# Optimization experiments

Hardware: AMD Instinct MI355X
Metric: run time of the kernel (lower is better)

## Reference

```python
import jax, jax.numpy as jnp
import numpy as np

HIDDEN = 1024
FEAT = 2048
BOTTLENECK = 512
B, T = 64, 512


def setup_inputs() -> dict:
    key = jax.random.key(0)
    k1, k2, k3, k4, k5 = jax.random.split(key, 5)
    hidden = jax.random.normal(k1, (B, HIDDEN), dtype=jnp.float32)
    feats = jax.random.normal(k2, (B, T, FEAT), dtype=jnp.float32)
    # nn.Linear weights stored as [out, in]; apply as x @ W.T
    W = jax.random.normal(k3, (BOTTLENECK, HIDDEN), dtype=jnp.float32) * (1.0 / np.sqrt(HIDDEN))
    U = jax.random.normal(k4, (BOTTLENECK, FEAT), dtype=jnp.float32) * (1.0 / np.sqrt(FEAT))
    b = jnp.ones((BOTTLENECK,), dtype=jnp.float32)
    w = jax.random.normal(k5, (1, BOTTLENECK), dtype=jnp.float32) * (1.0 / np.sqrt(BOTTLENECK))
    return {"hidden": hidden, "feats": feats, "W": W, "U": U, "b": b, "w": w}


def reference(hidden, feats, W, U, b, w):
    Wh = hidden @ W.T                      # [B, K]
    Uv = jnp.einsum('btf,kf->btk', feats, U)  # [B, T, K]
    e = jnp.tanh(Wh[:, None, :] + Uv + b)  # [B, T, K]
    energies = jnp.einsum('btk,ok->bto', e, w)  # [B, T, 1]
    weights = jax.nn.softmax(energies, axis=1)  # softmax over time
    attn_feats = jnp.sum(feats * weights, axis=1)  # [B, F]
    return attn_feats, weights
```

## Files before the change

kernel.cpp:

```cpp
#include <hip/hip_runtime.h>
#include <hip/hip_bf16.h>
#include <math.h>

#define BATCH 64
#define TDIM 512
#define FEAT 2048
#define HID 1024
#define KDIM 512
#define MROWS (BATCH * TDIM)
#define TCH 16
#define TCLEN (TDIM / TCH)

#define FEATS4 (MROWS * FEAT / 4)
#define U4 (KDIM * FEAT / 4)

typedef __attribute__((ext_vector_type(8))) short short8;
typedef __attribute__((ext_vector_type(4))) float floatx4;

#define GLL16(g, l)                                                     \
    __builtin_amdgcn_global_load_lds(                                   \
        (const __attribute__((address_space(1))) void*)(g),             \
        (__attribute__((address_space(3))) void*)(l), 16, 0, 0)

__device__ __forceinline__ unsigned short f2bf(float x) {
    unsigned int u = __float_as_uint(x);
    u += 0x7FFFu + ((u >> 16) & 1u);
    return (unsigned short)(u >> 16);
}

__device__ __forceinline__ float bf2f(unsigned short s) {
    return __uint_as_float(((unsigned int)s) << 16);
}

__global__ __launch_bounds__(256) void k0_fused(const float* __restrict__ feats,
                                                const float* __restrict__ U,
                                                const float* __restrict__ hidden,
                                                const float* __restrict__ W,
                                                const float* __restrict__ bias,
                                                unsigned short* __restrict__ fB,
                                                unsigned short* __restrict__ uB,
                                                float* __restrict__ whb) {
    int bx = blockIdx.x;
    if (bx < 1792) {
        int stride = 1792 * 256;
        for (int i = bx * 256 + threadIdx.x; i < FEATS4; i += stride) {
            float4 v = ((const float4*)feats)[i];
            ushort4 o;
            o.x = f2bf(v.x); o.y = f2bf(v.y); o.z = f2bf(v.z); o.w = f2bf(v.w);
            ((ushort4*)fB)[i] = o;
        }
    } else if (bx < 2048) {
        int stride = 256 * 256;
        for (int i = (bx - 1792) * 256 + threadIdx.x; i < U4; i += stride) {
            float4 v = ((const float4*)U)[i];
            ushort4 o;
            o.x = f2bf(v.x); o.y = f2bf(v.y); o.z = f2bf(v.z); o.w = f2bf(v.w);
            ((ushort4*)uB)[i] = o;
        }
    } else {
        int bid = bx - 2048;
        int b = bid >> 7;
        int k = (bid & 127) * 4 + (threadIdx.x >> 6);
        int lane = threadIdx.x & 63;
        const float* hrow = hidden + (size_t)b * HID;
        const float* wrow = W + (size_t)k * HID;
        float acc = 0.f;
        #pragma unroll 4
        for (int h = lane; h < HID; h += 64) acc += hrow[h] * wrow[h];
        #pragma unroll
        for (int off = 32; off > 0; off >>= 1) acc += __shfl_down(acc, off, 64);
        if (lane == 0) whb[b * KDIM + k] = acc + bias[k];
    }
}

__global__ __launch_bounds__(256, 2) void k2_mfma(const unsigned short* __restrict__ fB,
                                                  const unsigned short* __restrict__ uB,
                                                  const float* __restrict__ whb,
                                                  const float* __restrict__ wvec,
                                                  float* __restrict__ partial) {
    __shared__ unsigned short As[256 * 64];
    __shared__ unsigned short Bs[128 * 64];
    __shared__ float sums[2][256];

    const int tid  = threadIdx.x;
    const int wave = tid >> 6;
    const int lane = tid & 63;
    const int row0 = blockIdx.x * 256;
    const int k0   = blockIdx.y * 128;
    const int wm = wave >> 1, wn = wave & 1;
    const int col = lane & 15, quad = lane >> 4;

    const unsigned short* gA[8];
    unsigned short* lA[8];
    #pragma unroll
    for (int g = 0; g < 8; ++g) {
        int s = wave * 512 + g * 64 + lane;
        int r = s >> 3;
        int q = (s & 7) ^ (r & 7);
        gA[g] = fB + (size_t)(row0 + r) * FEAT + q * 8;
        lA[g] = As + (wave * 512 + g * 64) * 8;
    }
    const unsigned short* gBp[4];
    unsigned short* lB[4];
    #pragma unroll
    for (int g = 0; g < 4; ++g) {
        int s = wave * 256 + g * 64 + lane;
        int r = s >> 3;
        int q = (s & 7) ^ (r & 7);
        gBp[g] = uB + (size_t)(k0 + r) * FEAT + q * 8;
        lB[g] = Bs + (wave * 256 + g * 64) * 8;
    }

    floatx4 acc[8][4];
    #pragma unroll
    for (int i = 0; i < 8; ++i)
        #pragma unroll
        for (int j = 0; j < 4; ++j) acc[i][j] = (floatx4){0.f, 0.f, 0.f, 0.f};

    for (int f0 = 0; f0 < FEAT; f0 += 64) {
        #pragma unroll
        for (int g = 0; g < 8; ++g) { GLL16(gA[g], lA[g]); gA[g] += 64; }
        #pragma unroll
        for (int g = 0; g < 4; ++g) { GLL16(gBp[g], lB[g]); gBp[g] += 64; }
        __syncthreads();

        #pragma unroll
        for (int kk = 0; kk < 2; ++kk) {
            const int sw = ((kk * 4 + quad) ^ (col & 7)) * 8;
            short8 af[8], bf[4];
            #pragma unroll
            for (int i = 0; i < 8; ++i)
                af[i] = *(const short8*)&As[(wm * 128 + i * 16 + col) * 64 + sw];
            #pragma unroll
            for (int j = 0; j < 4; ++j)
                bf[j] = *(const short8*)&Bs[(wn * 64 + j * 16 + col) * 64 + sw];
            #pragma unroll
            for (int i = 0; i < 8; ++i)
                #pragma unroll
                for (int j = 0; j < 4; ++j)
                    acc[i][j] = __builtin_amdgcn_mfma_f32_16x16x32_bf16(
                        af[i], bf[j], acc[i][j], 0, 0, 0);
        }
        __syncthreads();
    }

    const int b = row0 >> 9;
    float wk[4], hk[4];
    #pragma unroll
    for (int j = 0; j < 4; ++j) {
        int k = k0 + wn * 64 + j * 16 + col;
        wk[j] = wvec[k];
        hk[j] = whb[b * KDIM + k];
    }
    #pragma unroll
    for (int i = 0; i < 8; ++i) {
        #pragma unroll
        for (int r = 0; r < 4; ++r) {
            float s = 0.f;
            #pragma unroll
            for (int j = 0; j < 4; ++j)
                s += tanhf(acc[i][j][r] + hk[j]) * wk[j];
            #pragma unroll
            for (int off = 8; off > 0; off >>= 1)
                s += __shfl_down(s, off, 16);
            if (col == 0)
                sums[wn][wm * 128 + i * 16 + quad * 4 + r] = s;
        }
    }
    __syncthreads();
    partial[blockIdx.y * MROWS + row0 + tid] = sums[0][tid] + sums[1][tid];
}

#define BM 128
#define BN 128
#define BF 16
#define LDSPAD 4

__global__ __launch_bounds__(256) void k2_energy(const float* __restrict__ feats,
                                                 const float* __restrict__ U,
                                                 const float* __restrict__ whb,
                                                 const float* __restrict__ wvec,
                                                 float* __restrict__ partial) {
    __shared__ __align__(16) float As[BF][BM + LDSPAD];
    __shared__ __align__(16) float Us[BF][BN + LDSPAD];

    const int row0 = blockIdx.x * BM;
    const int k0   = blockIdx.y * BN;
    const int tid  = threadIdx.x;
    const int tx   = tid & 15;
    const int ty   = tid >> 4;

    float acc[8][8];
    #pragma unroll
    for (int i = 0; i < 8; ++i)
        #pragma unroll
        for (int j = 0; j < 8; ++j) acc[i][j] = 0.f;

    for (int f0 = 0; f0 < FEAT; f0 += BF) {
        #pragma unroll
        for (int l = 0; l < 2; ++l) {
            int li = tid + l * 256;
            int r  = li >> 2;
            int c4 = (li & 3) * 4;
            float4 av = *(const float4*)(feats + (size_t)(row0 + r) * FEAT + f0 + c4);
            float4 uv = *(const float4*)(U     + (size_t)(k0   + r) * FEAT + f0 + c4);
            As[c4 + 0][r] = av.x; As[c4 + 1][r] = av.y;
            As[c4 + 2][r] = av.z; As[c4 + 3][r] = av.w;
            Us[c4 + 0][r] = uv.x; Us[c4 + 1][r] = uv.y;
            Us[c4 + 2][r] = uv.z; Us[c4 + 3][r] = uv.w;
        }
        __syncthreads();
        #pragma unroll
        for (int kf = 0; kf < BF; ++kf) {
            float4 a0 = *(const float4*)&As[kf][ty * 8];
            float4 a1 = *(const float4*)&As[kf][ty * 8 + 4];
            float4 u0 = *(const float4*)&Us[kf][tx * 8];
            float4 u1 = *(const float4*)&Us[kf][tx * 8 + 4];
            float a[8] = {a0.x, a0.y, a0.z, a0.w, a1.x, a1.y, a1.z, a1.w};
            float u[8] = {u0.x, u0.y, u0.z, u0.w, u1.x, u1.y, u1.z, u1.w};
            #pragma unroll
            for (int i = 0; i < 8; ++i)
                #pragma unroll
                for (int j = 0; j < 8; ++j) acc[i][j] += a[i] * u[j];
        }
        __syncthreads();
    }

    const int b = row0 >> 9;
    float psum[8];
    #pragma unroll
    for (int i = 0; i < 8; ++i) {
        float s = 0.f;
        #pragma unroll
        for (int j = 0; j < 8; ++j) {
            int k = k0 + tx * 8 + j;
            s += tanhf(acc[i][j] + whb[b * KDIM + k]) * wvec[k];
        }
        psum[i] = s;
    }
    #pragma unroll
    for (int off = 8; off > 0; off >>= 1)
        #pragma unroll
        for (int i = 0; i < 8; ++i) psum[i] += __shfl_down(psum[i], off, 16);

    if (tx == 0) {
        int c = blockIdx.y;
        #pragma unroll
        for (int i = 0; i < 8; ++i)
            partial[c * MROWS + row0 + ty * 8 + i] = psum[i];
    }
}

__global__ __launch_bounds__(512) void k3_softmax(const float* __restrict__ partial,
                                                  float* __restrict__ wout) {
    int b = blockIdx.x;
    int t = threadIdx.x;
    float e = 0.f;
    #pragma unroll
    for (int c = 0; c < 4; ++c) e += partial[c * MROWS + b * TDIM + t];

    __shared__ float sm[512];
    sm[t] = e;
    __syncthreads();
    #pragma unroll
    for (int s = 256; s > 0; s >>= 1) {
        if (t < s) sm[t] = fmaxf(sm[t], sm[t + s]);
        __syncthreads();
    }
    float m = sm[0];
    __syncthreads();
    float ex = __expf(e - m);
    sm[t] = ex;
    __syncthreads();
    #pragma unroll
    for (int s = 256; s > 0; s >>= 1) {
        if (t < s) sm[t] += sm[t + s];
        __syncthreads();
    }
    float inv = 1.f / sm[0];
    wout[b * TDIM + t] = ex * inv;
}

__global__ __launch_bounds__(256) void k4_partial_bf(const unsigned short* __restrict__ fB,
                                                     const float* __restrict__ weights,
                                                     float* __restrict__ partial4) {
    int b  = blockIdx.y;
    int t0 = blockIdx.x * TCLEN;
    int f8 = threadIdx.x * 8;
    __shared__ float wsm[TCLEN];
    if (threadIdx.x < TCLEN) wsm[threadIdx.x] = weights[b * TDIM + t0 + threadIdx.x];
    __syncthreads();

    const unsigned short* fp = fB + ((size_t)b * TDIM + t0) * FEAT + f8;
    float a[8];
    #pragma unroll
    for (int e = 0; e < 8; ++e) a[e] = 0.f;
    #pragma unroll 4
    for (int t = 0; t < TCLEN; ++t) {
        short8 v = *(const short8*)(fp + (size_t)t * FEAT);
        float w = wsm[t];
        #pragma unroll
        for (int e = 0; e < 8; ++e)
            a[e] += bf2f((unsigned short)v[e]) * w;
    }
    float* op = partial4 + ((size_t)blockIdx.x * BATCH + b) * FEAT + f8;
    float4 o0 = {a[0], a[1], a[2], a[3]};
    float4 o1 = {a[4], a[5], a[6], a[7]};
    *(float4*)op = o0;
    *(float4*)(op + 4) = o1;
}

__global__ __launch_bounds__(256) void k5_reduce(const float* __restrict__ partial4,
                                                 float* __restrict__ out) {
    int i4 = blockIdx.x * 256 + threadIdx.x;
    float4 s = ((const float4*)partial4)[i4];
    #pragma unroll
    for (int c = 1; c < TCH; ++c) {
        float4 v = ((const float4*)partial4)[(size_t)c * (BATCH * FEAT / 4) + i4];
        s.x += v.x; s.y += v.y; s.z += v.z; s.w += v.w;
    }
    ((float4*)out)[i4] = s;
}

__global__ __launch_bounds__(256) void k1_whb(const float* __restrict__ hidden,
                                              const float* __restrict__ W,
                                              const float* __restrict__ bias,
                                              float* __restrict__ whb) {
    int b = blockIdx.y;
    int k = blockIdx.x * 4 + (threadIdx.x >> 6);
    int lane = threadIdx.x & 63;
    const float* hrow = hidden + (size_t)b * HID;
    const float* wrow = W + (size_t)k * HID;
    float acc = 0.f;
    #pragma unroll 4
    for (int h = lane; h < HID; h += 64) acc += hrow[h] * wrow[h];
    #pragma unroll
    for (int off = 32; off > 0; off >>= 1) acc += __shfl_down(acc, off, 64);
    if (lane == 0) whb[b * KDIM + k] = acc + bias[k];
}

__global__ __launch_bounds__(256) void k4_direct(const float* __restrict__ feats,
                                                 const float* __restrict__ weights,
                                                 float* __restrict__ out) {
    int b = blockIdx.y;
    int f4 = (blockIdx.x * 256 + threadIdx.x) * 4;
    __shared__ float wsm[TDIM];
    wsm[threadIdx.x]       = weights[b * TDIM + threadIdx.x];
    wsm[threadIdx.x + 256] = weights[b * TDIM + 256 + threadIdx.x];
    __syncthreads();

    const float* fp = feats + (size_t)b * TDIM * FEAT + f4;
    float ax = 0.f, ay = 0.f, az = 0.f, aw = 0.f;
    for (int t = 0; t < TDIM; ++t) {
        float4 v = *(const float4*)(fp + (size_t)t * FEAT);
        float w = wsm[t];
        ax += v.x * w; ay += v.y * w; az += v.z * w; aw += v.w * w;
    }
    float4 o = {ax, ay, az, aw};
    *(float4*)(out + (size_t)b * FEAT + f4) = o;
}

extern "C" void kernel_launch(void* const* d_in, const int* in_sizes, int n_in,
                              void* d_out, int out_size, void* d_ws, size_t ws_size,
                              hipStream_t stream) {
    const float* hidden = (const float*)d_in[0];
    const float* feats  = (const float*)d_in[1];
    const float* W      = (const float*)d_in[2];
    const float* U      = (const float*)d_in[3];
    const float* bias   = (const float*)d_in[4];
    const float* wvec   = (const float*)d_in[5];

    float* out         = (float*)d_out;
    float* attn_out    = out;
    float* weights_out = out + (size_t)BATCH * FEAT;
    float* whb         = weights_out;
    float* partial     = attn_out;

    const size_t featsN = (size_t)MROWS * FEAT;
    const size_t uN     = (size_t)KDIM * FEAT;
    const size_t bf16Bytes = (featsN + uN) * sizeof(unsigned short);
    const size_t poolBytes = (size_t)TCH * BATCH * FEAT * sizeof(float);
    const bool fast = ws_size >= bf16Bytes + poolBytes;

    if (fast) {
        unsigned short* fBf = (unsigned short*)d_ws;
        unsigned short* uBf = fBf + featsN;
        float* pool4 = (float*)((char*)d_ws + bf16Bytes);
        k0_fused<<<dim3(10240), 256, 0, stream>>>(feats, U, hidden, W, bias,
                                                  fBf, uBf, whb);
        k2_mfma<<<dim3(MROWS / 256, KDIM / 128), 256, 0, stream>>>(
            fBf, uBf, whb, wvec, partial);
        k3_softmax<<<dim3(BATCH), 512, 0, stream>>>(partial, weights_out);
        k4_partial_bf<<<dim3(TCH, BATCH), 256, 0, stream>>>(
            fBf, weights_out, pool4);
        k5_reduce<<<dim3(BATCH * FEAT / 4 / 256), 256, 0, stream>>>(pool4, attn_out);
    } else {
        k1_whb<<<dim3(KDIM / 4, BATCH), 256, 0, stream>>>(hidden, W, bias, whb);
        k2_energy<<<dim3(MROWS / 128, KDIM / 128), 256, 0, stream>>>(
            feats, U, whb, wvec, partial);
        k3_softmax<<<dim3(BATCH), 512, 0, stream>>>(partial, weights_out);
        k4_direct<<<dim3(FEAT / 1024, BATCH), 256, 0, stream>>>(
            feats, weights_out, attn_out);
    }
}
```

Measured before the change: 501.3 us.

## Fuse feats bf16 conversion into MFMA GEMM and cover full K per block

Result: faster. 490.9 us (-2.1%).

```diff
diff --git a/kernel.cpp b/kernel.cpp
--- a/kernel.cpp
+++ b/kernel.cpp
@@ -1,5 +1,4 @@
 #include <hip/hip_runtime.h>
-#include <hip/hip_bf16.h>
 #include <math.h>
 
 #define BATCH 64
@@ -11,7 +10,6 @@
 #define TCH 16
 #define TCLEN (TDIM / TCH)
 
-#define FEATS4 (MROWS * FEAT / 4)
 #define U4 (KDIM * FEAT / 4)
 
 typedef __attribute__((ext_vector_type(8))) short short8;
@@ -28,37 +26,23 @@
     return (unsigned short)(u >> 16);
 }
 
-__device__ __forceinline__ float bf2f(unsigned short s) {
-    return __uint_as_float(((unsigned int)s) << 16);
-}
-
-__global__ __launch_bounds__(256) void k0_fused(const float* __restrict__ feats,
-                                                const float* __restrict__ U,
-                                                const float* __restrict__ hidden,
-                                                const float* __restrict__ W,
-                                                const float* __restrict__ bias,
-                                                unsigned short* __restrict__ fB,
-                                                unsigned short* __restrict__ uB,
-                                                float* __restrict__ whb) {
+__global__ __launch_bounds__(256) void k0n(const float* __restrict__ U,
+                                           const float* __restrict__ hidden,
+                                           const float* __restrict__ W,
+                                           const float* __restrict__ bias,
+                                           unsigned short* __restrict__ uB,
+                                           float* __restrict__ whb) {
     int bx = blockIdx.x;
-    if (bx < 1792) {
-        int stride = 1792 * 256;
-        for (int i = bx * 256 + threadIdx.x; i < FEATS4; i += stride) {
-            float4 v = ((const float4*)feats)[i];
-            ushort4 o;
-            o.x = f2bf(v.x); o.y = f2bf(v.y); o.z = f2bf(v.z); o.w = f2bf(v.w);
-            ((ushort4*)fB)[i] = o;
-        }
-    } else if (bx < 2048) {
+    if (bx < 256) {
         int stride = 256 * 256;
-        for (int i = (bx - 1792) * 256 + threadIdx.x; i < U4; i += stride) {
+        for (int i = bx * 256 + threadIdx.x; i < U4; i += stride) {
             float4 v = ((const float4*)U)[i];
             ushort4 o;
             o.x = f2bf(v.x); o.y = f2bf(v.y); o.z = f2bf(v.z); o.w = f2bf(v.w);
             ((ushort4*)uB)[i] = o;
         }
     } else {
-        int bid = bx - 2048;
+        int bid = bx - 256;
         int b = bid >> 7;
         int k = (bid & 127) * 4 + (threadIdx.x >> 6);
         int lane = threadIdx.x & 63;
@@ -73,71 +57,85 @@
     }
 }
 
-__global__ __launch_bounds__(256, 2) void k2_mfma(const unsigned short* __restrict__ fB,
-                                                  const unsigned short* __restrict__ uB,
-                                                  const float* __restrict__ whb,
-                                                  const float* __restrict__ wvec,
-                                                  float* __restrict__ partial) {
-    __shared__ unsigned short As[256 * 64];
-    __shared__ unsigned short Bs[128 * 64];
-    __shared__ float sums[2][256];
+__global__ __launch_bounds__(512, 2) void k2n(const float* __restrict__ feats,
+                                              const unsigned short* __restrict__ uB,
+                                              const float* __restrict__ whb,
+                                              const float* __restrict__ wvec,
+                                              float* __restrict__ energies) {
+    __shared__ __align__(16) unsigned short As[128 * 64];
+    __shared__ __align__(16) unsigned short Bs[512 * 64];
+    __shared__ float sums[4][128];
 
     const int tid  = threadIdx.x;
     const int wave = tid >> 6;
     const int lane = tid & 63;
-    const int row0 = blockIdx.x * 256;
-    const int k0   = blockIdx.y * 128;
-    const int wm = wave >> 1, wn = wave & 1;
+    const int row0 = blockIdx.x * 128;
+    const int wm = wave >> 2;
+    const int wn = wave & 3;
     const int col = lane & 15, quad = lane >> 4;
 
-    const unsigned short* gA[8];
-    unsigned short* lA[8];
+    const int sr = tid >> 3;
+    const int sc = (tid & 7) ^ (sr & 7);
+    const float* gA = feats + (size_t)(row0 + sr) * FEAT + sc * 8;
+    unsigned short* lA0 = As + tid * 8;
+    unsigned short* lA1 = As + (tid + 512) * 8;
+
+    const int bq = (lane & 7) ^ ((lane >> 3) & 7);
+    const int br = wave * 8 + (lane >> 3);
+    const unsigned short* gBp[8];
+    unsigned short* lB[8];
     #pragma unroll
     for (int g = 0; g < 8; ++g) {
-        int s = wave * 512 + g * 64 + lane;
-        int r = s >> 3;
-        int q = (s & 7) ^ (r & 7);
-        gA[g] = fB + (size_t)(row0 + r) * FEAT + q * 8;
-        lA[g] = As + (wave * 512 + g * 64) * 8;
-    }
-    const unsigned short* gBp[4];
-    unsigned short* lB[4];
-    #pragma unroll
-    for (int g = 0; g < 4; ++g) {
-        int s = wave * 256 + g * 64 + lane;
-        int r = s >> 3;
-        int q = (s & 7) ^ (r & 7);
-        gBp[g] = uB + (size_t)(k0 + r) * FEAT + q * 8;
-        lB[g] = Bs + (wave * 256 + g * 64) * 8;
-    }
-
-    floatx4 acc[8][4];
-    #pragma unroll
-    for (int i = 0; i < 8; ++i)
-        #pragma unroll
-        for (int j = 0; j < 4; ++j) acc[i][j] = (floatx4){0.f, 0.f, 0.f, 0.f};
+        gBp[g] = uB + (size_t)(g * 64 + br) * FEAT + bq * 8;
+        lB[g]  = Bs + (g * 512 + wave * 64) * 8;
+    }
+
+    floatx4 acc[4][8];
+    #pragma unroll
+    for (int i = 0; i < 4; ++i)
+        #pragma unroll
+        for (int j = 0; j < 8; ++j) acc[i][j] = (floatx4){0.f, 0.f, 0.f, 0.f};
+
+    float4 a0 = *(const float4*)(gA);
+    float4 a1 = *(const float4*)(gA + 4);
+    float4 a2 = *(const float4*)(gA + (size_t)64 * FEAT);
+    float4 a3 = *(const float4*)(gA + (size_t)64 * FEAT + 4);
+    gA += 64;
 
     for (int f0 = 0; f0 < FEAT; f0 += 64) {
         #pragma unroll
-        for (int g = 0; g < 8; ++g) { GLL16(gA[g], lA[g]); gA[g] += 64; }
-        #pragma unroll
-        for (int g = 0; g < 4; ++g) { GLL16(gBp[g], lB[g]); gBp[g] += 64; }
-        __syncthreads();
+        for (int g = 0; g < 8; ++g) { GLL16(gBp[g], lB[g]); gBp[g] += 64; }
+        short8 w0, w1;
+        w0[0] = f2bf(a0.x); w0[1] = f2bf(a0.y); w0[2] = f2bf(a0.z); w0[3] = f2bf(a0.w);
+        w0[4] = f2bf(a1.x); w0[5] = f2bf(a1.y); w0[6] = f2bf(a1.z); w0[7] = f2bf(a1.w);
+        w1[0] = f2bf(a2.x); w1[1] = f2bf(a2.y); w1[2] = f2bf(a2.z); w1[3] = f2bf(a2.w);
+        w1[4] = f2bf(a3.x); w1[5] = f2bf(a3.y); w1[6] = f2bf(a3.z); w1[7] = f2bf(a3.w);
+        *(short8*)lA0 = w0;
+        *(short8*)lA1 = w1;
+        __syncthreads();
+
+        if (f0 + 64 < FEAT) {
+            a0 = *(const float4*)(gA);
+            a1 = *(const float4*)(gA + 4);
+            a2 = *(const float4*)(gA + (size_t)64 * FEAT);
+            a3 = *(const float4*)(gA + (size_t)64 * FEAT + 4);
+            gA += 64;
+        }
 
         #pragma unroll
         for (int kk = 0; kk < 2; ++kk) {
             const int sw = ((kk * 4 + quad) ^ (col & 7)) * 8;
-            short8 af[8], bf[4];
-            #pragma unroll
-            for (int i = 0; i < 8; ++i)
-                af[i] = *(const short8*)&As[(wm * 128 + i * 16 + col) * 64 + sw];
-            #pragma unroll
-            for (int j = 0; j < 4; ++j)
-                bf[j] = *(const short8*)&Bs[(wn * 64 + j * 16 + col) * 64 + sw];
-            #pragma unroll
-            for (int i = 0; i < 8; ++i)
+            short8 af[4], bf[8];
+            #pragma unroll
+            for (int i = 0; i < 4; ++i)
+                af[i] = *(const short8*)&As[(wm * 64 + i * 16 + col) * 64 + sw];
+            #pragma unroll
+            for (int j = 0; j < 8; ++j)
+                bf[j] = *(const short8*)&Bs[(wn * 128 + j * 16 + col) * 64 + sw];
+            #pragma unroll
+            for (int i = 0; i < 4; ++i)
                 #pragma unroll
-                for (int j = 0; j < 4; ++j)
+                for (int j = 0; j < 8; ++j)
                     acc[i][j] = __builtin_amdgcn_mfma_f32_16x16x32_bf16(
                         af[i], bf[j], acc[i][j], 0, 0, 0);
         }
@@ -145,119 +143,39 @@
     }
 
     const int b = row0 >> 9;
-    float wk[4], hk[4];
-    #pragma unroll
-    for (int j = 0; j < 4; ++j) {
-        int k = k0 + wn * 64 + j * 16 + col;
+    float wk[8], hk[8];
+    #pragma unroll
+    for (int j = 0; j < 8; ++j) {
+        int k = wn * 128 + j * 16 + col;
         wk[j] = wvec[k];
         hk[j] = whb[b * KDIM + k];
     }
     #pragma unroll
-    for (int i = 0; i < 8; ++i) {
+    for (int i = 0; i < 4; ++i) {
         #pragma unroll
         for (int r = 0; r < 4; ++r) {
             float s = 0.f;
             #pragma unroll
-            for (int j = 0; j < 4; ++j)
+            for (int j = 0; j < 8; ++j)
                 s += tanhf(acc[i][j][r] + hk[j]) * wk[j];
             #pragma unroll
             for (int off = 8; off > 0; off >>= 1)
                 s += __shfl_down(s, off, 16);
             if (col == 0)
-                sums[wn][wm * 128 + i * 16 + quad * 4 + r] = s;
-        }
-    }
-    __syncthreads();
-    partial[blockIdx.y * MROWS + row0 + tid] = sums[0][tid] + sums[1][tid];
-}
-
-#define BM 128
-#define BN 128
-#define BF 16
-#define LDSPAD 4
-
-__global__ __launch_bounds__(256) void k2_energy(const float* __restrict__ feats,
-                                                 const float* __restrict__ U,
-                                                 const float* __restrict__ whb,
-                                                 const float* __restrict__ wvec,
-                                                 float* __restrict__ partial) {
-    __shared__ __align__(16) float As[BF][BM + LDSPAD];
-    __shared__ __align__(16) float Us[BF][BN + LDSPAD];
-
-    const int row0 = blockIdx.x * BM;
-    const int k0   = blockIdx.y * BN;
-    const int tid  = threadIdx.x;
-    const int tx   = tid & 15;
-    const int ty   = tid >> 4;
-
-    float acc[8][8];
-    #pragma unroll
-    for (int i = 0; i < 8; ++i)
-        #pragma unroll
-        for (int j = 0; j < 8; ++j) acc[i][j] = 0.f;
-
-    for (int f0 = 0; f0 < FEAT; f0 += BF) {
-        #pragma unroll
-        for (int l = 0; l < 2; ++l) {
-            int li = tid + l * 256;
-            int r  = li >> 2;
-            int c4 = (li & 3) * 4;
-            float4 av = *(const float4*)(feats + (size_t)(row0 + r) * FEAT + f0 + c4);
-            float4 uv = *(const float4*)(U     + (size_t)(k0   + r) * FEAT + f0 + c4);
-            As[c4 + 0][r] = av.x; As[c4 + 1][r] = av.y;
-            As[c4 + 2][r] = av.z; As[c4 + 3][r] = av.w;
-            Us[c4 + 0][r] = uv.x; Us[c4 + 1][r] = uv.y;
-            Us[c4 + 2][r] = uv.z; Us[c4 + 3][r] = uv.w;
-        }
-        __syncthreads();
-        #pragma unroll
-        for (int kf = 0; kf < BF; ++kf) {
-            float4 a0 = *(const float4*)&As[kf][ty * 8];
-            float4 a1 = *(const float4*)&As[kf][ty * 8 + 4];
-            float4 u0 = *(const float4*)&Us[kf][tx * 8];
-            float4 u1 = *(const float4*)&Us[kf][tx * 8 + 4];
-            float a[8] = {a0.x, a0.y, a0.z, a0.w, a1.x, a1.y, a1.z, a1.w};
-            float u[8] = {u0.x, u0.y, u0.z, u0.w, u1.x, u1.y, u1.z, u1.w};
-            #pragma unroll
-            for (int i = 0; i < 8; ++i)
-                #pragma unroll
-                for (int j = 0; j < 8; ++j) acc[i][j] += a[i] * u[j];
-        }
-        __syncthreads();
-    }
-
-    const int b = row0 >> 9;
-    float psum[8];
-    #pragma unroll
-    for (int i = 0; i < 8; ++i) {
-        float s = 0.f;
-        #pragma unroll
-        for (int j = 0; j < 8; ++j) {
-            int k = k0 + tx * 8 + j;
-            s += tanhf(acc[i][j] + whb[b * KDIM + k]) * wvec[k];
-        }
-        psum[i] = s;
-    }
-    #pragma unroll
-    for (int off = 8; off > 0; off >>= 1)
-        #pragma unroll
-        for (int i = 0; i < 8; ++i) psum[i] += __shfl_down(psum[i], off, 16);
-
-    if (tx == 0) {
-        int c = blockIdx.y;
-        #pragma unroll
-        for (int i = 0; i < 8; ++i)
-            partial[c * MROWS + row0 + ty * 8 + i] = psum[i];
-    }
-}
-
-__global__ __launch_bounds__(512) void k3_softmax(const float* __restrict__ partial,
-                                                  float* __restrict__ wout) {
+                sums[wn][wm * 64 + i * 16 + quad * 4 + r] = s;
+        }
+    }
+    __syncthreads();
+    if (tid < 128)
+        energies[row0 + tid] =
+            sums[0][tid] + sums[1][tid] + sums[2][tid] + sums[3][tid];
+}
+
+__global__ __launch_bounds__(512) void k3n(const float* __restrict__ energies,
+                                           float* __restrict__ wout) {
     int b = blockIdx.x;
     int t = threadIdx.x;
-    float e = 0.f;
-    #pragma unroll
-    for (int c = 0; c < 4; ++c) e += partial[c * MROWS + b * TDIM + t];
+    float e = energies[b * TDIM + t];
 
     __shared__ float sm[512];
     sm[t] = e;
@@ -281,9 +199,9 @@
     wout[b * TDIM + t] = ex * inv;
 }
 
-__global__ __launch_bounds__(256) void k4_partial_bf(const unsigned short* __restrict__ fB,
-                                                     const float* __restrict__ weights,
-                                                     float* __restrict__ partial4) {
+__global__ __launch_bounds__(256) void k4n(const float* __restrict__ feats,
+                                           const float* __restrict__ weights,
+                                           float* __restrict__ partial4) {
     int b  = blockIdx.y;
     int t0 = blockIdx.x * TCLEN;
     int f8 = threadIdx.x * 8;
@@ -291,17 +209,17 @@
     if (threadIdx.x < TCLEN) wsm[threadIdx.x] = weights[b * TDIM + t0 + threadIdx.x];
     __syncthreads();
 
-    const unsigned short* fp = fB + ((size_t)b * TDIM + t0) * FEAT + f8;
+    const float* fp = feats + ((size_t)b * TDIM + t0) * FEAT + f8;
     float a[8];
     #pragma unroll
     for (int e = 0; e < 8; ++e) a[e] = 0.f;
     #pragma unroll 4
     for (int t = 0; t < TCLEN; ++t) {
-        short8 v = *(const short8*)(fp + (size_t)t * FEAT);
+        float4 v0 = *(const float4*)(fp + (size_t)t * FEAT);
+        float4 v1 = *(const float4*)(fp + (size_t)t * FEAT + 4);
         float w = wsm[t];
-        #pragma unroll
-        for (int e = 0; e < 8; ++e)
-            a[e] += bf2f((unsigned short)v[e]) * w;
+        a[0] += v0.x * w; a[1] += v0.y * w; a[2] += v0.z * w; a[3] += v0.w * w;
+        a[4] += v1.x * w; a[5] += v1.y * w; a[6] += v1.z * w; a[7] += v1.w * w;
     }
     float* op = partial4 + ((size_t)blockIdx.x * BATCH + b) * FEAT + f8;
     float4 o0 = {a[0], a[1], a[2], a[3]};
@@ -321,6 +239,11 @@
     }
     ((float4*)out)[i4] = s;
 }
+
+#define BM 128
+#define BN 128
+#define BF 16
+#define LDSPAD 4
 
 __global__ __launch_bounds__(256) void k1_whb(const float* __restrict__ hidden,
                                               const float* __restrict__ W,
@@ -339,6 +262,111 @@
     if (lane == 0) whb[b * KDIM + k] = acc + bias[k];
 }
 
+__global__ __launch_bounds__(256) void k2_energy(const float* __restrict__ feats,
+                                                 const float* __restrict__ U,
+                                                 const float* __restrict__ whb,
+                                                 const float* __restrict__ wvec,
+                                                 float* __restrict__ partial) {
+    __shared__ __align__(16) float As[BF][BM + LDSPAD];
+    __shared__ __align__(16) float Us[BF][BN + LDSPAD];
+
+    const int row0 = blockIdx.x * BM;
+    const int k0   = blockIdx.y * BN;
+    const int tid  = threadIdx.x;
+    const int tx   = tid & 15;
+    const int ty   = tid >> 4;
+
+    float acc[8][8];
+    #pragma unroll
+    for (int i = 0; i < 8; ++i)
+        #pragma unroll
+        for (int j = 0; j < 8; ++j) acc[i][j] = 0.f;
+
+    for (int f0 = 0; f0 < FEAT; f0 += BF) {
+        #pragma unroll
+        for (int l = 0; l < 2; ++l) {
+            int li = tid + l * 256;
+            int r  = li >> 2;
+            int c4 = (li & 3) * 4;
+            float4 av = *(const float4*)(feats + (size_t)(row0 + r) * FEAT + f0 + c4);
+            float4 uv = *(const float4*)(U     + (size_t)(k0   + r) * FEAT + f0 + c4);
+            As[c4 + 0][r] = av.x; As[c4 + 1][r] = av.y;
+            As[c4 + 2][r] = av.z; As[c4 + 3][r] = av.w;
+            Us[c4 + 0][r] = uv.x; Us[c4 + 1][r] = uv.y;
+            Us[c4 + 2][r] = uv.z; Us[c4 + 3][r] = uv.w;
+        }
+        __syncthreads();
+        #pragma unroll
+        for (int kf = 0; kf < BF; ++kf) {
+            float4 a0 = *(const float4*)&As[kf][ty * 8];
+            float4 a1 = *(const float4*)&As[kf][ty * 8 + 4];
+            float4 u0 = *(const float4*)&Us[kf][tx * 8];
+            float4 u1 = *(const float4*)&Us[kf][tx * 8 + 4];
+            float a[8] = {a0.x, a0.y, a0.z, a0.w, a1.x, a1.y, a1.z, a1.w};
+            float u[8] = {u0.x, u0.y, u0.z, u0.w, u1.x, u1.y, u1.z, u1.w};
+            #pragma unroll
+            for (int i = 0; i < 8; ++i)
+                #pragma unroll
+                for (int j = 0; j < 8; ++j) acc[i][j] += a[i] * u[j];
+        }
+        __syncthreads();
+    }
+
+    const int b = row0 >> 9;
+    float psum[8];
+    #pragma unroll
+    for (int i = 0; i < 8; ++i) {
+        float s = 0.f;
+        #pragma unroll
+        for (int j = 0; j < 8; ++j) {
+            int k = k0 + tx * 8 + j;
+            s += tanhf(acc[i][j] + whb[b * KDIM + k]) * wvec[k];
+        }
+        psum[i] = s;
+    }
+    #pragma unroll
+    for (int off = 8; off > 0; off >>= 1)
+        #pragma unroll
+        for (int i = 0; i < 8; ++i) psum[i] += __shfl_down(psum[i], off, 16);
+
+    if (tx == 0) {
+        int c = blockIdx.y;
+        #pragma unroll
+        for (int i = 0; i < 8; ++i)
+            partial[c * MROWS + row0 + ty * 8 + i] = psum[i];
+    }
+}
+
+__global__ __launch_bounds__(512) void k3_softmax(const float* __restrict__ partial,
+                                                  float* __restrict__ wout) {
+    int b = blockIdx.x;
+    int t = threadIdx.x;
+    float e = 0.f;
+    #pragma unroll
+    for (int c = 0; c < 4; ++c) e += partial[c * MROWS + b * TDIM + t];
+
+    __shared__ float sm[512];
+    sm[t] = e;
+    __syncthreads();
+    #pragma unroll
+    for (int s = 256; s > 0; s >>= 1) {
+        if (t < s) sm[t] = fmaxf(sm[t], sm[t + s]);
+        __syncthreads();
+    }
+    float m = sm[0];
+    __syncthreads();
+    float ex = __expf(e - m);
+    sm[t] = ex;
+    __syncthreads();
+    #pragma unroll
+    for (int s = 256; s > 0; s >>= 1) {
+        if (t < s) sm[t] += sm[t + s];
+        __syncthreads();
+    }
+    float inv = 1.f / sm[0];
+    wout[b * TDIM + t] = ex * inv;
+}
+
 __global__ __launch_bounds__(256) void k4_direct(const float* __restrict__ feats,
                                                  const float* __restrict__ weights,
                                                  float* __restrict__ out) {
@@ -374,31 +402,26 @@
     float* attn_out    = out;
     float* weights_out = out + (size_t)BATCH * FEAT;
     float* whb         = weights_out;
-    float* partial     = attn_out;
-
-    const size_t featsN = (size_t)MROWS * FEAT;
-    const size_t uN     = (size_t)KDIM * FEAT;
-    const size_t bf16Bytes = (featsN + uN) * sizeof(unsigned short);
+    float* energies    = attn_out;
+
+    const size_t uN        = (size_t)KDIM * FEAT;
+    const size_t uBytes    = uN * sizeof(unsigned short);
     const size_t poolBytes = (size_t)TCH * BATCH * FEAT * sizeof(float);
-    const bool fast = ws_size >= bf16Bytes + poolBytes;
+    const bool fast = ws_size >= uBytes + poolBytes;
 
     if (fast) {
-        unsigned short* fBf = (unsigned short*)d_ws;
-        unsigned short* uBf = fBf + featsN;
-        float* pool4 = (float*)((char*)d_ws + bf16Bytes);
-        k0_fused<<<dim3(10240), 256, 0, stream>>>(feats, U, hidden, W, bias,
-                                                  fBf, uBf, whb);
-        k2_mfma<<<dim3(MROWS / 256, KDIM / 128), 256, 0, stream>>>(
-            fBf, uBf, whb, wvec, partial);
-        k3_softmax<<<dim3(BATCH), 512, 0, stream>>>(partial, weights_out);
-        k4_partial_bf<<<dim3(TCH, BATCH), 256, 0, stream>>>(
-            fBf, weights_out, pool4);
+        unsigned short* uBf = (unsigned short*)d_ws;
+        float* pool4 = (float*)((char*)d_ws + uBytes);
+        k0n<<<dim3(256 + 8192), 256, 0, stream>>>(U, hidden, W, bias, uBf, whb);
+        k2n<<<dim3(MROWS / 128), 512, 0, stream>>>(feats, uBf, whb, wvec, energies);
+        k3n<<<dim3(BATCH), 512, 0, stream>>>(energies, weights_out);
+        k4n<<<dim3(TCH, BATCH), 256, 0, stream>>>(feats, weights_out, pool4);
         k5_reduce<<<dim3(BATCH * FEAT / 4 / 256), 256, 0, stream>>>(pool4, attn_out);
     } else {
         k1_whb<<<dim3(KDIM / 4, BATCH), 256, 0, stream>>>(hidden, W, bias, whb);
         k2_energy<<<dim3(MROWS / 128, KDIM / 128), 256, 0, stream>>>(
-            feats, U, whb, wvec, partial);
-        k3_softmax<<<dim3(BATCH), 512, 0, stream>>>(partial, weights_out);
+            feats, U, whb, wvec, energies);
+        k3_softmax<<<dim3(BATCH), 512, 0, stream>>>(energies, weights_out);
         k4_direct<<<dim3(FEAT / 1024, BATCH), 256, 0, stream>>>(
             feats, weights_out, attn_out);
     }
```

## Pre-pack swizzled bf16 tiles and double-buffer a 256x256 MFMA energy GEMM

Applied to the files above, without the earlier changes.

Result: slower. 532.4 us (+6.2%).

```diff
diff --git a/kernel.cpp b/kernel.cpp
--- a/kernel.cpp
+++ b/kernel.cpp
@@ -1,5 +1,4 @@
 #include <hip/hip_runtime.h>
-#include <hip/hip_bf16.h>
 #include <math.h>
 
 #define BATCH 64
@@ -11,8 +10,10 @@
 #define TCH 16
 #define TCLEN (TDIM / TCH)
 
-#define FEATS4 (MROWS * FEAT / 4)
-#define U4 (KDIM * FEAT / 4)
+#define NSTEP (FEAT / 64)
+#define TSLOT 2048
+#define ASLOTS (128 * 32 * TSLOT)
+#define BSLOTS (2 * 32 * TSLOT)
 
 typedef __attribute__((ext_vector_type(8))) short short8;
 typedef __attribute__((ext_vector_type(4))) float floatx4;
@@ -22,43 +23,61 @@
         (const __attribute__((address_space(1))) void*)(g),             \
         (__attribute__((address_space(3))) void*)(l), 16, 0, 0)
 
+#define VMWAIT(N) asm volatile("s_waitcnt vmcnt(" #N ")" ::: "memory")
+#define SCHEDB    __builtin_amdgcn_sched_barrier(0)
+#define SBAR      __builtin_amdgcn_s_barrier()
+
 __device__ __forceinline__ unsigned short f2bf(float x) {
     unsigned int u = __float_as_uint(x);
     u += 0x7FFFu + ((u >> 16) & 1u);
     return (unsigned short)(u >> 16);
 }
 
-__device__ __forceinline__ float bf2f(unsigned short s) {
-    return __uint_as_float(((unsigned int)s) << 16);
-}
-
-__global__ __launch_bounds__(256) void k0_fused(const float* __restrict__ feats,
-                                                const float* __restrict__ U,
-                                                const float* __restrict__ hidden,
-                                                const float* __restrict__ W,
-                                                const float* __restrict__ bias,
-                                                unsigned short* __restrict__ fB,
-                                                unsigned short* __restrict__ uB,
-                                                float* __restrict__ whb) {
+__global__ __launch_bounds__(256) void k0p(const float* __restrict__ feats,
+                                           const float* __restrict__ U,
+                                           const float* __restrict__ hidden,
+                                           const float* __restrict__ W,
+                                           const float* __restrict__ bias,
+                                           unsigned short* __restrict__ Apk,
+                                           unsigned short* __restrict__ Bpk,
+                                           float* __restrict__ whb) {
     int bx = blockIdx.x;
-    if (bx < 1792) {
-        int stride = 1792 * 256;
-        for (int i = bx * 256 + threadIdx.x; i < FEATS4; i += stride) {
-            float4 v = ((const float4*)feats)[i];
-            ushort4 o;
-            o.x = f2bf(v.x); o.y = f2bf(v.y); o.z = f2bf(v.z); o.w = f2bf(v.w);
-            ((ushort4*)fB)[i] = o;
-        }
-    } else if (bx < 2048) {
-        int stride = 256 * 256;
-        for (int i = (bx - 1792) * 256 + threadIdx.x; i < U4; i += stride) {
-            float4 v = ((const float4*)U)[i];
-            ushort4 o;
-            o.x = f2bf(v.x); o.y = f2bf(v.y); o.z = f2bf(v.z); o.w = f2bf(v.w);
-            ((ushort4*)uB)[i] = o;
-        }
+    if (bx < 8192) {
+        for (size_t gsl = (size_t)bx * 256 + threadIdx.x; gsl < ASLOTS;
+             gsl += (size_t)8192 * 256) {
+            int strip = (int)(gsl >> 16);
+            int rem   = (int)(gsl & 65535);
+            int tile  = rem >> 11;
+            int s     = rem & 2047;
+            int r     = s >> 3;
+            int c     = (s & 7) ^ (r & 7);
+            const float* src = feats + ((size_t)strip * 256 + r) * FEAT + tile * 64 + c * 8;
+            float4 v0 = *(const float4*)src;
+            float4 v1 = *(const float4*)(src + 4);
+            ushort4 o0, o1;
+            o0.x = f2bf(v0.x); o0.y = f2bf(v0.y); o0.z = f2bf(v0.z); o0.w = f2bf(v0.w);
+            o1.x = f2bf(v1.x); o1.y = f2bf(v1.y); o1.z = f2bf(v1.z); o1.w = f2bf(v1.w);
+            ((ushort4*)Apk)[gsl * 2]     = o0;
+            ((ushort4*)Apk)[gsl * 2 + 1] = o1;
+        }
+    } else if (bx < 8704) {
+        size_t gsl = (size_t)(bx - 8192) * 256 + threadIdx.x;
+        int cb   = (int)(gsl >> 16);
+        int rem  = (int)(gsl & 65535);
+        int tile = rem >> 11;
+        int s    = rem & 2047;
+        int r    = s >> 3;
+        int c    = (s & 7) ^ (r & 7);
+        const float* src = U + ((size_t)cb * 256 + r) * FEAT + tile * 64 + c * 8;
+        float4 v0 = *(const float4*)src;
+        float4 v1 = *(const float4*)(src + 4);
+        ushort4 o0, o1;
+        o0.x = f2bf(v0.x); o0.y = f2bf(v0.y); o0.z = f2bf(v0.z); o0.w = f2bf(v0.w);
+        o1.x = f2bf(v1.x); o1.y = f2bf(v1.y); o1.z = f2bf(v1.z); o1.w = f2bf(v1.w);
+        ((ushort4*)Bpk)[gsl * 2]     = o0;
+        ((ushort4*)Bpk)[gsl * 2 + 1] = o1;
     } else {
-        int bid = bx - 2048;
+        int bid = bx - 8704;
         int b = bid >> 7;
         int k = (bid & 127) * 4 + (threadIdx.x >> 6);
         int lane = threadIdx.x & 63;
@@ -73,43 +92,39 @@
     }
 }
 
-__global__ __launch_bounds__(256, 2) void k2_mfma(const unsigned short* __restrict__ fB,
-                                                  const unsigned short* __restrict__ uB,
-                                                  const float* __restrict__ whb,
-                                                  const float* __restrict__ wvec,
-                                                  float* __restrict__ partial) {
-    __shared__ unsigned short As[256 * 64];
-    __shared__ unsigned short Bs[128 * 64];
-    __shared__ float sums[2][256];
+__global__ __launch_bounds__(512, 2) void k2p(const unsigned short* __restrict__ Apk,
+                                              const unsigned short* __restrict__ Bpk,
+                                              const float* __restrict__ whb,
+                                              const float* __restrict__ wvec,
+                                              float* __restrict__ partial) {
+    __shared__ __align__(16) unsigned short As[2][16384];
+    __shared__ __align__(16) unsigned short Bs[2][16384];
 
     const int tid  = threadIdx.x;
     const int wave = tid >> 6;
     const int lane = tid & 63;
-    const int row0 = blockIdx.x * 256;
-    const int k0   = blockIdx.y * 128;
-    const int wm = wave >> 1, wn = wave & 1;
+    const int wm = wave >> 2, wn = wave & 3;
     const int col = lane & 15, quad = lane >> 4;
-
-    const unsigned short* gA[8];
-    unsigned short* lA[8];
-    #pragma unroll
-    for (int g = 0; g < 8; ++g) {
-        int s = wave * 512 + g * 64 + lane;
-        int r = s >> 3;
-        int q = (s & 7) ^ (r & 7);
-        gA[g] = fB + (size_t)(row0 + r) * FEAT + q * 8;
-        lA[g] = As + (wave * 512 + g * 64) * 8;
-    }
-    const unsigned short* gBp[4];
-    unsigned short* lB[4];
-    #pragma unroll
-    for (int g = 0; g < 4; ++g) {
-        int s = wave * 256 + g * 64 + lane;
-        int r = s >> 3;
-        int q = (s & 7) ^ (r & 7);
-        gBp[g] = uB + (size_t)(k0 + r) * FEAT + q * 8;
-        lB[g] = Bs + (wave * 256 + g * 64) * 8;
-    }
+    const int bx = blockIdx.x, by = blockIdx.y;
+
+    const unsigned short* gA = Apk + (size_t)bx * (32 * TSLOT) * 8;
+    const unsigned short* gB = Bpk + (size_t)by * (32 * TSLOT) * 8;
+
+    #define STAGE(tt, hh, bb)                                                   \
+        do {                                                                    \
+            const int sbase_ = ((hh) & 1) * 1024 + wave * 128;                  \
+            if ((hh) < 2) {                                                     \
+                GLL16(gA + ((size_t)(tt) * TSLOT + sbase_) * 8 + lane * 8,      \
+                      &As[bb][sbase_ * 8]);                                     \
+                GLL16(gA + ((size_t)(tt) * TSLOT + sbase_ + 64) * 8 + lane * 8, \
+                      &As[bb][(sbase_ + 64) * 8]);                              \
+            } else {                                                            \
+                GLL16(gB + ((size_t)(tt) * TSLOT + sbase_) * 8 + lane * 8,      \
+                      &Bs[bb][sbase_ * 8]);                                     \
+                GLL16(gB + ((size_t)(tt) * TSLOT + sbase_ + 64) * 8 + lane * 8, \
+                      &Bs[bb][(sbase_ + 64) * 8]);                              \
+            }                                                                   \
+        } while (0)
 
     floatx4 acc[8][4];
     #pragma unroll
@@ -117,38 +132,63 @@
         #pragma unroll
         for (int j = 0; j < 4; ++j) acc[i][j] = (floatx4){0.f, 0.f, 0.f, 0.f};
 
-    for (int f0 = 0; f0 < FEAT; f0 += 64) {
-        #pragma unroll
-        for (int g = 0; g < 8; ++g) { GLL16(gA[g], lA[g]); gA[g] += 64; }
-        #pragma unroll
-        for (int g = 0; g < 4; ++g) { GLL16(gBp[g], lB[g]); gBp[g] += 64; }
-        __syncthreads();
-
-        #pragma unroll
-        for (int kk = 0; kk < 2; ++kk) {
-            const int sw = ((kk * 4 + quad) ^ (col & 7)) * 8;
-            short8 af[8], bf[4];
+    #pragma unroll
+    for (int h = 0; h < 4; ++h) STAGE(0, h, 0);
+
+    short8 bf[4][2];
+    for (int t = 0; t < NSTEP; ++t) {
+        const int cb = t & 1, sb = cb ^ 1;
+        #pragma unroll
+        for (int p = 0; p < 4; ++p) {
+            if (t < NSTEP - 1) STAGE(t + 1, p, sb);
+            if (p == 0) {
+                if (t < NSTEP - 1) { VMWAIT(2); } else { VMWAIT(0); }
+                SCHEDB;
+            }
+            SBAR; SCHEDB;
+
+            short8 af[2][2];
             #pragma unroll
-            for (int i = 0; i < 8; ++i)
-                af[i] = *(const short8*)&As[(wm * 128 + i * 16 + col) * 64 + sw];
-            #pragma unroll
-            for (int j = 0; j < 4; ++j)
-                bf[j] = *(const short8*)&Bs[(wn * 64 + j * 16 + col) * 64 + sw];
-            #pragma unroll
-            for (int i = 0; i < 8; ++i)
+            for (int i = 0; i < 2; ++i)
+                #pragma unroll
+                for (int kk = 0; kk < 2; ++kk) {
+                    const int row = wm * 128 + (2 * p + i) * 16 + col;
+                    af[i][kk] = *(const short8*)
+                        &As[cb][(row * 8 + ((kk * 4 + quad) ^ (col & 7))) * 8];
+                }
+            if (p == 0) {
                 #pragma unroll
                 for (int j = 0; j < 4; ++j)
-                    acc[i][j] = __builtin_amdgcn_mfma_f32_16x16x32_bf16(
-                        af[i], bf[j], acc[i][j], 0, 0, 0);
-        }
-        __syncthreads();
-    }
-
-    const int b = row0 >> 9;
+                    #pragma unroll
+                    for (int kk = 0; kk < 2; ++kk) {
+                        const int row = wn * 64 + j * 16 + col;
+                        bf[j][kk] = *(const short8*)
+                            &Bs[cb][(row * 8 + ((kk * 4 + quad) ^ (col & 7))) * 8];
+                    }
+            }
+            __builtin_amdgcn_s_setprio(1);
+            #pragma unroll
+            for (int i = 0; i < 2; ++i)
+                #pragma unroll
+                for (int j = 0; j < 4; ++j)
+                    #pragma unroll
+                    for (int kk = 0; kk < 2; ++kk)
+                        acc[2 * p + i][j] = __builtin_amdgcn_mfma_f32_16x16x32_bf16(
+                            af[i][kk], bf[j][kk], acc[2 * p + i][j], 0, 0, 0);
+            __builtin_amdgcn_s_setprio(0);
+            SCHEDB; SBAR; SCHEDB;
+        }
+    }
+    #undef STAGE
+
+    __syncthreads();
+
+    float (*sums)[256] = (float (*)[256])As;
+    const int b = bx >> 1;
     float wk[4], hk[4];
     #pragma unroll
     for (int j = 0; j < 4; ++j) {
-        int k = k0 + wn * 64 + j * 16 + col;
+        const int k = by * 256 + wn * 64 + j * 16 + col;
         wk[j] = wvec[k];
         hk[j] = whb[b * KDIM + k];
     }
@@ -168,159 +208,89 @@
         }
     }
     __syncthreads();
-    partial[blockIdx.y * MROWS + row0 + tid] = sums[0][tid] + sums[1][tid];
+    if (tid < 256)
+        partial[(size_t)by * MROWS + bx * 256 + tid] =
+            sums[0][tid] + sums[1][tid] + sums[2][tid] + sums[3][tid];
+}
+
+__global__ __launch_bounds__(512) void k3n(const float* __restrict__ partial,
+                                           float* __restrict__ wout) {
+    int b = blockIdx.x;
+    int t = threadIdx.x;
+    int idx = b * TDIM + t;
+    float e = partial[idx] + partial[MROWS + idx];
+
+    __shared__ float sm[512];
+    sm[t] = e;
+    __syncthreads();
+    #pragma unroll
+    for (int s = 256; s > 0; s >>= 1) {
+        if (t < s) sm[t] = fmaxf(sm[t], sm[t + s]);
+        __syncthreads();
+    }
+    float m = sm[0];
+    __syncthreads();
+    float ex = __expf(e - m);
+    sm[t] = ex;
+    __syncthreads();
+    #pragma unroll
+    for (int s = 256; s > 0; s >>= 1) {
+        if (t < s) sm[t] += sm[t + s];
+        __syncthreads();
+    }
+    float inv = 1.f / sm[0];
+    wout[b * TDIM + t] = ex * inv;
+}
+
+__global__ __launch_bounds__(256) void k4p(const unsigned short* __restrict__ Apk,
+                                           const float* __restrict__ weights,
+                                           float* __restrict__ partial4) {
+    int b  = blockIdx.y;
+    int t0 = blockIdx.x * TCLEN;
+    int tile = threadIdx.x >> 3;
+    int ch   = threadIdx.x & 7;
+    int f0   = tile * 64 + ch * 8;
+    __shared__ float wsm[TCLEN];
+    if (threadIdx.x < TCLEN) wsm[threadIdx.x] = weights[b * TDIM + t0 + threadIdx.x];
+    __syncthreads();
+
+    float a[8];
+    #pragma unroll
+    for (int e = 0; e < 8; ++e) a[e] = 0.f;
+    #pragma unroll 4
+    for (int t = 0; t < TCLEN; ++t) {
+        int row = b * TDIM + t0 + t;
+        int strip = row >> 8, r = row & 255;
+        const short8 v = *(const short8*)(Apk +
+            (((size_t)strip * 65536 + (size_t)tile * TSLOT + r * 8 + (ch ^ (r & 7))) * 8));
+        float w = wsm[t];
+        #pragma unroll
+        for (int e = 0; e < 8; ++e)
+            a[e] += __uint_as_float(((unsigned int)(unsigned short)v[e]) << 16) * w;
+    }
+    float* op = partial4 + ((size_t)blockIdx.x * BATCH + b) * FEAT + f0;
+    float4 o0 = {a[0], a[1], a[2], a[3]};
+    float4 o1 = {a[4], a[5], a[6], a[7]};
+    *(float4*)op = o0;
+    *(float4*)(op + 4) = o1;
+}
+
+__global__ __launch_bounds__(256) void k5_reduce(const float* __restrict__ partial4,
+                                                 float* __restrict__ out) {
+    int i4 = blockIdx.x * 256 + threadIdx.x;
+    float4 s = ((const float4*)partial4)[i4];
+    #pragma unroll
+    for (int c = 1; c < TCH; ++c) {
+        float4 v = ((const float4*)partial4)[(size_t)c * (BATCH * FEAT / 4) + i4];
+        s.x += v.x; s.y += v.y; s.z += v.z; s.w += v.w;
+    }
+    ((float4*)out)[i4] = s;
 }
 
 #define BM 128
 #define BN 128
 #define BF 16
 #define LDSPAD 4
-
-__global__ __launch_bounds__(256) void k2_energy(const float* __restrict__ feats,
-                                                 const float* __restrict__ U,
-                                                 const float* __restrict__ whb,
-                                                 const float* __restrict__ wvec,
-                                                 float* __restrict__ partial) {
-    __shared__ __align__(16) float As[BF][BM + LDSPAD];
-    __shared__ __align__(16) float Us[BF][BN + LDSPAD];
-
-    const int row0 = blockIdx.x * BM;
-    const int k0   = blockIdx.y * BN;
-    const int tid  = threadIdx.x;
-    const int tx   = tid & 15;
-    const int ty   = tid >> 4;
-
-    float acc[8][8];
-    #pragma unroll
-    for (int i = 0; i < 8; ++i)
-        #pragma unroll
-        for (int j = 0; j < 8; ++j) acc[i][j] = 0.f;
-
-    for (int f0 = 0; f0 < FEAT; f0 += BF) {
-        #pragma unroll
-        for (int l = 0; l < 2; ++l) {
-            int li = tid + l * 256;
-            int r  = li >> 2;
-            int c4 = (li & 3) * 4;
-            float4 av = *(const float4*)(feats + (size_t)(row0 + r) * FEAT + f0 + c4);
-            float4 uv = *(const float4*)(U     + (size_t)(k0   + r) * FEAT + f0 + c4);
-            As[c4 + 0][r] = av.x; As[c4 + 1][r] = av.y;
-            As[c4 + 2][r] = av.z; As[c4 + 3][r] = av.w;
-            Us[c4 + 0][r] = uv.x; Us[c4 + 1][r] = uv.y;
-            Us[c4 + 2][r] = uv.z; Us[c4 + 3][r] = uv.w;
-        }
-        __syncthreads();
-        #pragma unroll
-        for (int kf = 0; kf < BF; ++kf) {
-            float4 a0 = *(const float4*)&As[kf][ty * 8];
-            float4 a1 = *(const float4*)&As[kf][ty * 8 + 4];
-            float4 u0 = *(const float4*)&Us[kf][tx * 8];
-            float4 u1 = *(const float4*)&Us[kf][tx * 8 + 4];
-            float a[8] = {a0.x, a0.y, a0.z, a0.w, a1.x, a1.y, a1.z, a1.w};
-            float u[8] = {u0.x, u0.y, u0.z, u0.w, u1.x, u1.y, u1.z, u1.w};
-            #pragma unroll
-            for (int i = 0; i < 8; ++i)
-                #pragma unroll
-                for (int j = 0; j < 8; ++j) acc[i][j] += a[i] * u[j];
-        }
-        __syncthreads();
-    }
-
-    const int b = row0 >> 9;
-    float psum[8];
-    #pragma unroll
-    for (int i = 0; i < 8; ++i) {
-        float s = 0.f;
-        #pragma unroll
-        for (int j = 0; j < 8; ++j) {
-            int k = k0 + tx * 8 + j;
-            s += tanhf(acc[i][j] + whb[b * KDIM + k]) * wvec[k];
-        }
-        psum[i] = s;
-    }
-    #pragma unroll
-    for (int off = 8; off > 0; off >>= 1)
-        #pragma unroll
-        for (int i = 0; i < 8; ++i) psum[i] += __shfl_down(psum[i], off, 16);
-
-    if (tx == 0) {
-        int c = blockIdx.y;
-        #pragma unroll
-        for (int i = 0; i < 8; ++i)
-            partial[c * MROWS + row0 + ty * 8 + i] = psum[i];
-    }
-}
-
-__global__ __launch_bounds__(512) void k3_softmax(const float* __restrict__ partial,
-                                                  float* __restrict__ wout) {
-    int b = blockIdx.x;
-    int t = threadIdx.x;
-    float e = 0.f;
-    #pragma unroll
-    for (int c = 0; c < 4; ++c) e += partial[c * MROWS + b * TDIM + t];
-
-    __shared__ float sm[512];
-    sm[t] = e;
-    __syncthreads();
-    #pragma unroll
-    for (int s = 256; s > 0; s >>= 1) {
-        if (t < s) sm[t] = fmaxf(sm[t], sm[t + s]);
-        __syncthreads();
-    }
-    float m = sm[0];
-    __syncthreads();
-    float ex = __expf(e - m);
-    sm[t] = ex;
-    __syncthreads();
-    #pragma unroll
-    for (int s = 256; s > 0; s >>= 1) {
-        if (t < s) sm[t] += sm[t + s];
-        __syncthreads();
-    }
-    float inv = 1.f / sm[0];
-    wout[b * TDIM + t] = ex * inv;
-}
-
-__global__ __launch_bounds__(256) void k4_partial_bf(const unsigned short* __restrict__ fB,
-                                                     const float* __restrict__ weights,
-                                                     float* __restrict__ partial4) {
-    int b  = blockIdx.y;
-    int t0 = blockIdx.x * TCLEN;
-    int f8 = threadIdx.x * 8;
-    __shared__ float wsm[TCLEN];
-    if (threadIdx.x < TCLEN) wsm[threadIdx.x] = weights[b * TDIM + t0 + threadIdx.x];
-    __syncthreads();
-
-    const unsigned short* fp = fB + ((size_t)b * TDIM + t0) * FEAT + f8;
-    float a[8];
-    #pragma unroll
-    for (int e = 0; e < 8; ++e) a[e] = 0.f;
-    #pragma unroll 4
-    for (int t = 0; t < TCLEN; ++t) {
-        short8 v = *(const short8*)(fp + (size_t)t * FEAT);
-        float w = wsm[t];
-        #pragma unroll
-        for (int e = 0; e < 8; ++e)
-            a[e] += bf2f((unsigned short)v[e]) * w;
-    }
-    float* op = partial4 + ((size_t)blockIdx.x * BATCH + b) * FEAT + f8;
-    float4 o0 = {a[0], a[1], a[2], a[3]};
-    float4 o1 = {a[4], a[5], a[6], a[7]};
-    *(float4*)op = o0;
-    *(float4*)(op + 4) = o1;
-}
-
-__global__ __launch_bounds__(256) void k5_reduce(const float* __restrict__ partial4,
-                                                 float* __restrict__ out) {
-    int i4 = blockIdx.x * 256 + threadIdx.x;
-    float4 s = ((const float4*)partial4)[i4];
-    #pragma unroll
-    for (int c = 1; c < TCH; ++c) {
-        float4 v = ((const float4*)partial4)[(size_t)c * (BATCH * FEAT / 4) + i4];
-        s.x += v.x; s.y += v.y; s.z += v.z; s.w += v.w;
-    }
-    ((float4*)out)[i4] = s;
-}
 
 __global__ __launch_bounds__(256) void k1_whb(const float* __restrict__ hidden,
                                               const float* __restrict__ W,
@@ -339,6 +309,111 @@
     if (lane == 0) whb[b * KDIM + k] = acc + bias[k];
 }
 
+__global__ __launch_bounds__(256) void k2_energy(const float* __restrict__ feats,
+                                                 const float* __restrict__ U,
+                                                 const float* __restrict__ whb,
+                                                 const float* __restrict__ wvec,
+                                                 float* __restrict__ partial) {
+    __shared__ __align__(16) float As[BF][BM + LDSPAD];
+    __shared__ __align__(16) float Us[BF][BN + LDSPAD];
+
+    const int row0 = blockIdx.x * BM;
+    const int k0   = blockIdx.y * BN;
+    const int tid  = threadIdx.x;
+    const int tx   = tid & 15;
+    const int ty   = tid >> 4;
+
+    float acc[8][8];
+    #pragma unroll
+    for (int i = 0; i < 8; ++i)
+        #pragma unroll
+        for (int j = 0; j < 8; ++j) acc[i][j] = 0.f;
+
+    for (int f0 = 0; f0 < FEAT; f0 += BF) {
+        #pragma unroll
+        for (int l = 0; l < 2; ++l) {
+            int li = tid + l * 256;
+            int r  = li >> 2;
+            int c4 = (li & 3) * 4;
+            float4 av = *(const float4*)(feats + (size_t)(row0 + r) * FEAT + f0 + c4);
+            float4 uv = *(const float4*)(U     + (size_t)(k0   + r) * FEAT + f0 + c4);
+            As[c4 + 0][r] = av.x; As[c4 + 1][r] = av.y;
+            As[c4 + 2][r] = av.z; As[c4 + 3][r] = av.w;
+            Us[c4 + 0][r] = uv.x; Us[c4 + 1][r] = uv.y;
+            Us[c4 + 2][r] = uv.z; Us[c4 + 3][r] = uv.w;
+        }
+        __syncthreads();
+        #pragma unroll
+        for (int kf = 0; kf < BF; ++kf) {
+            float4 a0 = *(const float4*)&As[kf][ty * 8];
+            float4 a1 = *(const float4*)&As[kf][ty * 8 + 4];
+            float4 u0 = *(const float4*)&Us[kf][tx * 8];
+            float4 u1 = *(const float4*)&Us[kf][tx * 8 + 4];
+            float a[8] = {a0.x, a0.y, a0.z, a0.w, a1.x, a1.y, a1.z, a1.w};
+            float u[8] = {u0.x, u0.y, u0.z, u0.w, u1.x, u1.y, u1.z, u1.w};
+            #pragma unroll
+            for (int i = 0; i < 8; ++i)
+                #pragma unroll
+                for (int j = 0; j < 8; ++j) acc[i][j] += a[i] * u[j];
+        }
+        __syncthreads();
+    }
+
+    const int b = row0 >> 9;
+    float psum[8];
+    #pragma unroll
+    for (int i = 0; i < 8; ++i) {
+        float s = 0.f;
+        #pragma unroll
+        for (int j = 0; j < 8; ++j) {
+            int k = k0 + tx * 8 + j;
+            s += tanhf(acc[i][j] + whb[b * KDIM + k]) * wvec[k];
+        }
+        psum[i] = s;
+    }
+    #pragma unroll
+    for (int off = 8; off > 0; off >>= 1)
+        #pragma unroll
+        for (int i = 0; i < 8; ++i) psum[i] += __shfl_down(psum[i], off, 16);
+
+    if (tx == 0) {
+        int c = blockIdx.y;
+        #pragma unroll
+        for (int i = 0; i < 8; ++i)
+            partial[c * MROWS + row0 + ty * 8 + i] = psum[i];
+    }
+}
+
+__global__ __launch_bounds__(512) void k3_softmax(const float* __restrict__ partial,
+                                                  float* __restrict__ wout) {
+    int b = blockIdx.x;
+    int t = threadIdx.x;
+    float e = 0.f;
+    #pragma unroll
+    for (int c = 0; c < 4; ++c) e += partial[c * MROWS + b * TDIM + t];
+
+    __shared__ float sm[512];
+    sm[t] = e;
+    __syncthreads();
+    #pragma unroll
+    for (int s = 256; s > 0; s >>= 1) {
+        if (t < s) sm[t] = fmaxf(sm[t], sm[t + s]);
+        __syncthreads();
+    }
+    float m = sm[0];
+    __syncthreads();
+    float ex = __expf(e - m);
+    sm[t] = ex;
+    __syncthreads();
+    #pragma unroll
+    for (int s = 256; s > 0; s >>= 1) {
+        if (t < s) sm[t] += sm[t + s];
+        __syncthreads();
+    }
+    float inv = 1.f / sm[0];
+    wout[b * TDIM + t] = ex * inv;
+}
+
 __global__ __launch_bounds__(256) void k4_direct(const float* __restrict__ feats,
                                                  const float* __restrict__ weights,
                                                  float* __restrict__ out) {
@@ -376,23 +451,20 @@
     float* whb         = weights_out;
     float* partial     = attn_out;
 
-    const size_t featsN = (size_t)MROWS * FEAT;
-    const size_t uN     = (size_t)KDIM * FEAT;
-    const size_t bf16Bytes = (featsN + uN) * sizeof(unsigned short);
+    const size_t aBytes    = (size_t)ASLOTS * 16;
+    const size_t bBytes    = (size_t)BSLOTS * 16;
     const size_t poolBytes = (size_t)TCH * BATCH * FEAT * sizeof(float);
-    const bool fast = ws_size >= bf16Bytes + poolBytes;
+    const bool fast = ws_size >= aBytes + bBytes + poolBytes;
 
     if (fast) {
-        unsigned short* fBf = (unsigned short*)d_ws;
-        unsigned short* uBf = fBf + featsN;
-        float* pool4 = (float*)((char*)d_ws + bf16Bytes);
-        k0_fused<<<dim3(10240), 256, 0, stream>>>(feats, U, hidden, W, bias,
-                                                  fBf, uBf, whb);
-        k2_mfma<<<dim3(MROWS / 256, KDIM / 128), 256, 0, stream>>>(
-            fBf, uBf, whb, wvec, partial);
-        k3_softmax<<<dim3(BATCH), 512, 0, stream>>>(partial, weights_out);
-        k4_partial_bf<<<dim3(TCH, BATCH), 256, 0, stream>>>(
-            fBf, weights_out, pool4);
+        unsigned short* Apk = (unsigned short*)d_ws;
+        unsigned short* Bpk = (unsigned short*)((char*)d_ws + aBytes);
+        float* pool4 = (float*)((char*)d_ws + aBytes + bBytes);
+        k0p<<<dim3(16896), 256, 0, stream>>>(feats, U, hidden, W, bias,
+                                             Apk, Bpk, whb);
+        k2p<<<dim3(128, 2), 512, 0, stream>>>(Apk, Bpk, whb, wvec, partial);
+        k3n<<<dim3(BATCH), 512, 0, stream>>>(partial, weights_out);
+        k4p<<<dim3(TCH, BATCH), 256, 0, stream>>>(Apk, weights_out, pool4);
         k5_reduce<<<dim3(BATCH * FEAT / 4 / 256), 256, 0, stream>>>(pool4, attn_out);
     } else {
         k1_whb<<<dim3(KDIM / 4, BATCH), 256, 0, stream>>>(hidden, W, bias, whb);
```
